# Kernel optimization log

Hardware: AMD Instinct MI355X
Metric: run time of the kernel (lower is better)

Reference implementation:

```python
import jax, jax.numpy as jnp
import numpy as np


def setup_inputs() -> dict:
    key = jax.random.key(0)
    k1, k2 = jax.random.split(key)
    B, T, D, K = 16, 4096, 1024, 512
    h = jax.random.normal(k1, (B, T, D), dtype=jnp.float32)
    codebook = jax.random.normal(k2, (K, D), dtype=jnp.float32)
    return {"h": h, "codebook": codebook}


def reference(h, codebook):
    """SAMMCodebook.encode: nearest-codeword indices via squared L2 distance.

    h: [B, T, D]; codebook: [K, D] -> z: [B, T] int32
    """
    B, T, D = h.shape
    h_flat = h.reshape(-1, D)                                  # [N, D]
    h_sq = jnp.sum(h_flat * h_flat, axis=-1, keepdims=True)    # [N, 1]
    c_sq = jnp.sum(codebook * codebook, axis=-1)[None, :]      # [1, K]
    # dist[n,k] = ||h_n||^2 + ||c_k||^2 - 2 <h_n, c_k>
    dist = h_sq + c_sq - 2.0 * (h_flat @ codebook.T)           # [N, K]
    z = jnp.argmin(dist, axis=-1).reshape(B, T)
    return z.astype(jnp.int32)
```

## Files before the change

### kernel.cpp

```cpp
#include <hip/hip_runtime.h>


#define D_DIM 1024
#define K_CB  512
#define DELTA 4.0f
#define MAXC_IN 15
#define FULLSCAN 0xFFFFu

typedef __attribute__((ext_vector_type(8))) short short8;
typedef __attribute__((ext_vector_type(4))) float floatx4;

#define WS_CBB  0ull
#define WS_CSQ  1048576ull

typedef const unsigned int __attribute__((address_space(1)))* gaddr_t;
typedef unsigned int __attribute__((address_space(3)))* laddr_t;
static __device__ __forceinline__ void async_copy16(const void* g, void* l) {
    __builtin_amdgcn_global_load_lds((gaddr_t)g, (laddr_t)l, 16, 0, 0);
}

static __device__ __forceinline__ unsigned f2bf(float f) {
    unsigned u = __builtin_bit_cast(unsigned, f);
    return (u + 0x7FFFu + ((u >> 16) & 1u)) >> 16;
}

__global__ __launch_bounds__(256)
void prep_kernel(const float* __restrict__ cb, unsigned short* __restrict__ cbb,
                 float* __restrict__ csq) {
    __shared__ float red[4];
    const int k = blockIdx.x, t = threadIdx.x;
    const float4 v = *(const float4*)(cb + (size_t)k * D_DIM + t * 4);
    uint2 u;
    u.x = f2bf(v.x) | (f2bf(v.y) << 16);
    u.y = f2bf(v.z) | (f2bf(v.w) << 16);
    *(uint2*)(cbb + (size_t)k * D_DIM + t * 4) = u;
    float s = v.x * v.x + v.y * v.y + v.z * v.z + v.w * v.w;
    #pragma unroll
    for (int off = 32; off > 0; off >>= 1) s += __shfl_down(s, off, 64);
    if ((t & 63) == 0) red[t >> 6] = s;
    __syncthreads();
    if (t == 0) csq[k] = red[0] + red[1] + red[2] + red[3];
}

__global__ __launch_bounds__(256, 2)
void coarse_kernel(const float* __restrict__ h,
                   const unsigned short* __restrict__ cbb,
                   const float* __restrict__ csq,
                   const float* __restrict__ cb,
                   int* __restrict__ out) {
    __shared__ unsigned char smem[73728] __attribute__((aligned(16)));
    unsigned short* As = (unsigned short*)smem;
    unsigned short* Bs = (unsigned short*)(smem + 8192);

    const int tid = threadIdx.x;
    const int w = tid >> 6, lane = tid & 63;
    const int l15 = lane & 15, kq = lane >> 4;
    const size_t row0 = (size_t)blockIdx.x * 64;
    const int wc_ = w * 128;

    const int qp8 = (kq ^ ((l15 >> 1) & 3)) * 8;

    const int ar = tid >> 2, aql = tid & 3;
    const float* gA = h + (row0 + ar) * D_DIM + aql * 8;
    const int awoff = ar * 32 + (aql ^ ((ar >> 1) & 3)) * 8;

    const int qsrc = (tid & 3) ^ ((tid >> 3) & 3);
    const unsigned char* cbb_b = (const unsigned char*)cbb;
    const size_t bsrc0 = ((size_t)(tid >> 2) * D_DIM + qsrc * 8) * 2;

    floatx4 acc[4][8];
    #pragma unroll
    for (int i = 0; i < 4; ++i)
        #pragma unroll
        for (int j = 0; j < 8; ++j) acc[i][j] = (floatx4){0.f, 0.f, 0.f, 0.f};

    {
        const floatx4 va0 = __builtin_nontemporal_load((const floatx4*)gA);
        const floatx4 va1 = __builtin_nontemporal_load((const floatx4*)(gA + 4));
        #pragma unroll
        for (int j = 0; j < 8; ++j)
            async_copy16(cbb_b + bsrc0 + (size_t)j * 64 * D_DIM * 2,
                         Bs + (size_t)j * 2048 + w * 512);
        uint4 u;
        u.x = f2bf(va0.x) | (f2bf(va0.y) << 16);
        u.y = f2bf(va0.z) | (f2bf(va0.w) << 16);
        u.z = f2bf(va1.x) | (f2bf(va1.y) << 16);
        u.w = f2bf(va1.z) | (f2bf(va1.w) << 16);
        *(uint4*)(As + awoff) = u;
        __syncthreads();
    }

    int cur = 0;
    for (int s = 0; s < 32; ++s) {
        floatx4 vb0, vb1;
        const int dn = (s + 1) * 32;
        if (s < 31) {
            vb0 = __builtin_nontemporal_load((const floatx4*)(gA + dn));
            vb1 = __builtin_nontemporal_load((const floatx4*)(gA + dn + 4));
            #pragma unroll
            for (int j = 0; j < 8; ++j)
                async_copy16(cbb_b + bsrc0 + (size_t)j * 64 * D_DIM * 2 + (size_t)dn * 2,
                             Bs + (cur ^ 1) * 16384 + (size_t)j * 2048 + w * 512);
        }

        const unsigned short* Asc = As + cur * 2048;
        const unsigned short* Bsc = Bs + cur * 16384;
        short8 a[4], b[8];
        #pragma unroll
        for (int rt = 0; rt < 4; ++rt)
            a[rt] = *(const short8*)(Asc + (rt * 16 + l15) * 32 + qp8);
        #pragma unroll
        for (int ct = 0; ct < 8; ++ct)
            b[ct] = *(const short8*)(Bsc + (wc_ + ct * 16 + l15) * 32 + qp8);
        #pragma unroll
        for (int rt = 0; rt < 4; ++rt)
            #pragma unroll
            for (int ct = 0; ct < 8; ++ct)
                acc[rt][ct] = __builtin_amdgcn_mfma_f32_16x16x32_bf16(
                    a[rt], b[ct], acc[rt][ct], 0, 0, 0);

        if (s < 31) {
            uint4 u;
            u.x = f2bf(vb0.x) | (f2bf(vb0.y) << 16);
            u.y = f2bf(vb0.z) | (f2bf(vb0.w) << 16);
            u.z = f2bf(vb1.x) | (f2bf(vb1.y) << 16);
            u.w = f2bf(vb1.z) | (f2bf(vb1.w) << 16);
            *(uint4*)(As + (cur ^ 1) * 2048 + awoff) = u;
        }
        __syncthreads();
        cur ^= 1;
    }

    float k1[16], k2[16];
    unsigned cpk[16];
    #pragma unroll
    for (int i = 0; i < 16; ++i) { k1[i] = 3.4e38f; k2[i] = 3.4e38f; cpk[i] = 0; }
    #pragma unroll
    for (int ct = 0; ct < 8; ++ct) {
        const int col = wc_ + ct * 16 + l15;
        const float cq = csq[col];
        #pragma unroll
        for (int rt = 0; rt < 4; ++rt)
            #pragma unroll
            for (int reg = 0; reg < 4; ++reg) {
                const float s = fmaf(-2.0f, acc[rt][ct][reg], cq);
                const int ri = rt * 4 + reg;
                if (s < k1[ri]) {
                    k2[ri] = k1[ri]; k1[ri] = s;
                    cpk[ri] = (cpk[ri] << 16) | (unsigned)col;
                } else if (s < k2[ri]) {
                    k2[ri] = s;
                    cpk[ri] = (cpk[ri] & 0xFFFFu) | ((unsigned)col << 16);
                }
            }
    }

    float* mval = (float*)smem;
    int*   mcol = (int*)(smem + 33024);
    unsigned short* ccnt  = (unsigned short*)(smem + 66048);
    unsigned short* clist = (unsigned short*)(smem + 66176);
    __syncthreads();
    #pragma unroll
    for (int rt = 0; rt < 4; ++rt)
        #pragma unroll
        for (int reg = 0; reg < 4; ++reg) {
            const int ri = rt * 4 + reg;
            const int r = rt * 16 + kq * 4 + reg;
            const int e = (w * 16 + l15) * 2;
            mval[r * 129 + e] = k1[ri];
            mcol[r * 129 + e] = (int)(cpk[ri] & 0xFFFFu);
            mval[r * 129 + e + 1] = k2[ri];
            mcol[r * 129 + e + 1] = (int)(cpk[ri] >> 16);
        }
    __syncthreads();

    if (tid < 64) {
        const int r = tid;
        float bv = mval[r * 129]; int bc = mcol[r * 129];
        for (int e = 1; e < 128; ++e) {
            const float v = mval[r * 129 + e];
            const int   c = mcol[r * 129 + e];
            if (v < bv || (v == bv && c < bc)) { bv = v; bc = c; }
        }
        const float thr = bv + DELTA;
        int others = 0;
        for (int e = 0; e < 128; ++e) {
            const float v = mval[r * 129 + e];
            const int   c = mcol[r * 129 + e];
            if (v < thr && c != bc) {
                if (others < MAXC_IN) clist[r * 16 + 1 + others] = (unsigned short)c;
                ++others;
            }
        }
        if (others == 0) {
            out[row0 + r] = bc;
            ccnt[r] = 0;
        } else if (others <= MAXC_IN) {
            clist[r * 16] = (unsigned short)bc;
            ccnt[r] = (unsigned short)(others + 1);
        } else {
            ccnt[r] = (unsigned short)FULLSCAN;
        }
    }
    __syncthreads();

    for (int r = w; r < 64; r += 4) {
        const unsigned cnt = ccnt[r];
        if (cnt == 0) continue;
        const size_t grow = row0 + r;
        const float* hrow = h + grow * D_DIM;
        float4 hv[4];
        #pragma unroll
        for (int j = 0; j < 4; ++j)
            hv[j] = *(const float4*)(hrow + j * 256 + lane * 4);
        float bs = 3.4e38f; int bc = 0x7fffffff;
        const bool full = (cnt == FULLSCAN);
        const int total = full ? K_CB : (int)cnt;
        for (int i = 0; i < total; ++i) {
            const int c = full ? i : (int)clist[r * 16 + i];
            const float* crow = cb + (size_t)c * D_DIM;
            float d = 0.0f;
            #pragma unroll
            for (int j = 0; j < 4; ++j) {
                const float4 cv = *(const float4*)(crow + j * 256 + lane * 4);
                d = fmaf(hv[j].x, cv.x, d);
                d = fmaf(hv[j].y, cv.y, d);
                d = fmaf(hv[j].z, cv.z, d);
                d = fmaf(hv[j].w, cv.w, d);
            }
            #pragma unroll
            for (int off = 32; off > 0; off >>= 1) d += __shfl_down(d, off, 64);
            d = __shfl(d, 0, 64);
            const float sc = fmaf(-2.0f, d, csq[c]);
            if (sc < bs || (sc == bs && c < bc)) { bs = sc; bc = c; }
        }
        if (lane == 0) out[grow] = bc;
    }
}

extern "C" void kernel_launch(void* const* d_in, const int* in_sizes, int n_in,
                              void* d_out, int out_size, void* d_ws, size_t ws_size,
                              hipStream_t stream) {
    const float* h  = (const float*)d_in[0];
    const float* cb = (const float*)d_in[1];
    int* out = (int*)d_out;
    unsigned char* ws = (unsigned char*)d_ws;
    const int nrows = in_sizes[0] / D_DIM;

    unsigned short* cbb = (unsigned short*)(ws + WS_CBB);
    float* csq = (float*)(ws + WS_CSQ);

    prep_kernel<<<dim3(K_CB), dim3(256), 0, stream>>>(cb, cbb, csq);
    coarse_kernel<<<dim3(nrows / 64), dim3(256), 0, stream>>>(
        h, cbb, csq, cb, out);
}
```

Before: 482.6 us.

## Restructure main loop: per-wave private B staging, chunked A staging, fewer barriers

Each wave now loads only its own 128 codebook rows into LDS, so B tiles are waited on with s_waitcnt vmcnt per wave instead of a block-wide barrier each k-step. The activation tile is staged 128 columns at a time with a new XOR swizzle, cutting __syncthreads from 32 to about 16 per block. MFMA sections are raised in priority with s_setprio. LDS use grows, which could affect the two-blocks-per-CU occupancy, and the A loads are no longer overlapped with compute.

```diff
diff --git a/kernel.cpp b/kernel.cpp
--- a/kernel.cpp
+++ b/kernel.cpp
@@ -48,9 +48,9 @@
                    const float* __restrict__ csq,
                    const float* __restrict__ cb,
                    int* __restrict__ out) {
-    __shared__ unsigned char smem[73728] __attribute__((aligned(16)));
+    __shared__ unsigned char smem[81920] __attribute__((aligned(16)));
     unsigned short* As = (unsigned short*)smem;
-    unsigned short* Bs = (unsigned short*)(smem + 8192);
+    unsigned short* Bs = (unsigned short*)(smem + 16384);
 
     const int tid = threadIdx.x;
     const int w = tid >> 6, lane = tid & 63;
@@ -60,13 +60,14 @@
 
     const int qp8 = (kq ^ ((l15 >> 1) & 3)) * 8;
 
-    const int ar = tid >> 2, aql = tid & 3;
-    const float* gA = h + (row0 + ar) * D_DIM + aql * 8;
-    const int awoff = ar * 32 + (aql ^ ((ar >> 1) & 3)) * 8;
-
-    const int qsrc = (tid & 3) ^ ((tid >> 3) & 3);
+    const int qsrc = (lane & 3) ^ ((lane >> 3) & 3);
+    const int brow = w * 128 + (lane >> 2);
     const unsigned char* cbb_b = (const unsigned char*)cbb;
-    const size_t bsrc0 = ((size_t)(tid >> 2) * D_DIM + qsrc * 8) * 2;
+    const size_t bsrc_base = ((size_t)brow * D_DIM + qsrc * 8) * 2;
+
+    const int ar = tid >> 2, aq4 = (tid & 3) * 4;
+    const float* gA = h + (row0 + ar) * D_DIM + (tid & 3) * 32;
+    const int aswz = l15 & 7;
 
     floatx4 acc[4][8];
     #pragma unroll
@@ -74,62 +75,79 @@
         #pragma unroll
         for (int j = 0; j < 8; ++j) acc[i][j] = (floatx4){0.f, 0.f, 0.f, 0.f};
 
+#define ISSUE_B(dkn, par) \
+    _Pragma("unroll") \
+    for (int j = 0; j < 8; ++j) \
+        async_copy16(cbb_b + bsrc_base + (size_t)j * (16 * D_DIM * 2) + (size_t)(dkn) * 2, \
+                     Bs + (par) * 16384 + (w * 128 + j * 16) * 32);
+
+#define STAGE_A(cc) do { \
+    floatx4 av[8]; \
+    _Pragma("unroll") \
+    for (int k = 0; k < 8; ++k) \
+        av[k] = __builtin_nontemporal_load((const floatx4*)(gA + (cc) * 128 + k * 4)); \
+    _Pragma("unroll") \
+    for (int j = 0; j < 4; ++j) { \
+        uint4 u; \
+        u.x = f2bf(av[2 * j].x)     | (f2bf(av[2 * j].y) << 16); \
+        u.y = f2bf(av[2 * j].z)     | (f2bf(av[2 * j].w) << 16); \
+        u.z = f2bf(av[2 * j + 1].x) | (f2bf(av[2 * j + 1].y) << 16); \
+        u.w = f2bf(av[2 * j + 1].z) | (f2bf(av[2 * j + 1].w) << 16); \
+        const int ps = (aq4 + j) ^ (ar & 7); \
+        *(uint4*)(As + ar * 128 + ps * 8) = u; \
+    } \
+} while (0)
+
+#define INNER_STEP(ii, PF) do { \
+    if (PF) { \
+        ISSUE_B((c4 + (ii) + 1) * 32, ((ii) + 1) & 1); \
+        asm volatile("s_waitcnt vmcnt(8)" ::: "memory"); \
+    } else { \
+        asm volatile("s_waitcnt vmcnt(0)" ::: "memory"); \
+    } \
+    __builtin_amdgcn_sched_barrier(0); \
+    short8 a[4], b[8]; \
+    _Pragma("unroll") \
+    for (int rt = 0; rt < 4; ++rt) \
+        a[rt] = *(const short8*)(As + (rt * 16 + l15) * 128 + ((((ii) * 4 + kq)) ^ aswz) * 8); \
+    _Pragma("unroll") \
+    for (int ct = 0; ct < 8; ++ct) \
+        b[ct] = *(const short8*)(Bs + ((ii) & 1) * 16384 + (wc_ + ct * 16 + l15) * 32 + qp8); \
+    __builtin_amdgcn_s_setprio(1); \
+    _Pragma("unroll") \
+    for (int rt = 0; rt < 4; ++rt) \
+        _Pragma("unroll") \
+        for (int ct = 0; ct < 8; ++ct) \
+            acc[rt][ct] = __builtin_amdgcn_mfma_f32_16x16x32_bf16( \
+                a[rt], b[ct], acc[rt][ct], 0, 0, 0); \
+    __builtin_amdgcn_s_setprio(0); \
+} while (0)
+
+    ISSUE_B(0, 0);
+
+    for (int c = 0; c < 7; ++c) {
+        const int c4 = c * 4;
+        STAGE_A(c);
+        __syncthreads();
+        INNER_STEP(0, true);
+        INNER_STEP(1, true);
+        INNER_STEP(2, true);
+        INNER_STEP(3, true);
+        __syncthreads();
+    }
     {
-        const floatx4 va0 = __builtin_nontemporal_load((const floatx4*)gA);
-        const floatx4 va1 = __builtin_nontemporal_load((const floatx4*)(gA + 4));
-        #pragma unroll
-        for (int j = 0; j < 8; ++j)
-            async_copy16(cbb_b + bsrc0 + (size_t)j * 64 * D_DIM * 2,
-                         Bs + (size_t)j * 2048 + w * 512);
-        uint4 u;
-        u.x = f2bf(va0.x) | (f2bf(va0.y) << 16);
-        u.y = f2bf(va0.z) | (f2bf(va0.w) << 16);
-        u.z = f2bf(va1.x) | (f2bf(va1.y) << 16);
-        u.w = f2bf(va1.z) | (f2bf(va1.w) << 16);
-        *(uint4*)(As + awoff) = u;
+        const int c4 = 28;
+        STAGE_A(7);
         __syncthreads();
-    }
-
-    int cur = 0;
-    for (int s = 0; s < 32; ++s) {
-        floatx4 vb0, vb1;
-        const int dn = (s + 1) * 32;
-        if (s < 31) {
-            vb0 = __builtin_nontemporal_load((const floatx4*)(gA + dn));
-            vb1 = __builtin_nontemporal_load((const floatx4*)(gA + dn + 4));
-            #pragma unroll
-            for (int j = 0; j < 8; ++j)
-                async_copy16(cbb_b + bsrc0 + (size_t)j * 64 * D_DIM * 2 + (size_t)dn * 2,
-                             Bs + (cur ^ 1) * 16384 + (size_t)j * 2048 + w * 512);
-        }
-
-        const unsigned short* Asc = As + cur * 2048;
-        const unsigned short* Bsc = Bs + cur * 16384;
-        short8 a[4], b[8];
-        #pragma unroll
-        for (int rt = 0; rt < 4; ++rt)
-            a[rt] = *(const short8*)(Asc + (rt * 16 + l15) * 32 + qp8);
-        #pragma unroll
-        for (int ct = 0; ct < 8; ++ct)
-            b[ct] = *(const short8*)(Bsc + (wc_ + ct * 16 + l15) * 32 + qp8);
-        #pragma unroll
-        for (int rt = 0; rt < 4; ++rt)
-            #pragma unroll
-            for (int ct = 0; ct < 8; ++ct)
-                acc[rt][ct] = __builtin_amdgcn_mfma_f32_16x16x32_bf16(
-                    a[rt], b[ct], acc[rt][ct], 0, 0, 0);
-
-        if (s < 31) {
-            uint4 u;
-            u.x = f2bf(vb0.x) | (f2bf(vb0.y) << 16);
-            u.y = f2bf(vb0.z) | (f2bf(vb0.w) << 16);
-            u.z = f2bf(vb1.x) | (f2bf(vb1.y) << 16);
-            u.w = f2bf(vb1.z) | (f2bf(vb1.w) << 16);
-            *(uint4*)(As + (cur ^ 1) * 2048 + awoff) = u;
-        }
-        __syncthreads();
-        cur ^= 1;
-    }
+        INNER_STEP(0, true);
+        INNER_STEP(1, true);
+        INNER_STEP(2, true);
+        INNER_STEP(3, false);
+    }
+
+#undef INNER_STEP
+#undef STAGE_A
+#undef ISSUE_B
 
     float k1[16], k2[16];
     unsigned cpk[16];
```

New measurement: 512.7 us. +6.2%, slower.
